# Performance work log

Measured on AMD Instinct MI355X. Metric: run time of the kernel, lower is better.

Reference implementation:

```python
import jax, jax.numpy as jnp
import numpy as np

NA, T, NUM_CIRC = 192, 80, 5
BUFFER_DIST = 0.25


def setup_inputs() -> dict:
    key = jax.random.key(0)
    k1, k2 = jax.random.split(key, 2)
    rng = np.random.default_rng(0)
    # veh_att: UNNORMALIZED (length, width) per agent
    L = rng.uniform(3.5, 5.5, NA).astype(np.float32)
    W = rng.uniform(1.6, 2.2, NA).astype(np.float32)
    rad = W / 2.0
    cent_min = -(L / 2.0) + rad
    cent_max = (L / 2.0) - rad
    # linspace of circle centers along x axis of each vehicle, (NA, num_circ)
    frac = np.linspace(0.0, 1.0, NUM_CIRC, dtype=np.float32)[None, :]
    cent_x = cent_min[:, None] + frac * (cent_max - cent_min)[:, None]
    centroids = np.stack(
        [cent_x, np.zeros_like(cent_x), np.ones_like(cent_x), np.zeros_like(cent_x)],
        axis=2,
    ).astype(np.float32)  # (NA, num_circ, 4)
    penalty_dists = (rad[:, None] + rad[None, :] + BUFFER_DIST).astype(np.float32)
    off_diag_mask = ~np.eye(NA, dtype=bool)  # single scene graph (ptr=None)
    # traj: (NA, T, 4) = (x, y, hx, hy), unnormalized world coords
    pos = jax.random.uniform(k1, (NA, T, 2), minval=-100.0, maxval=100.0)
    head = jax.random.normal(k2, (NA, T, 2))
    traj = jnp.concatenate([pos, head], axis=-1).astype(jnp.float32)
    return {
        "traj": traj,
        "centroids": jnp.asarray(centroids),
        "penalty_dists": jnp.asarray(penalty_dists),
        "off_diag_mask": jnp.asarray(off_diag_mask),
    }


def reference(traj, centroids, penalty_dists, off_diag_mask):
    # traj: (NA, T, 4); centroids: (NA, C, 4); penalty_dists/off_diag_mask: (NA, NA)
    na, t, _ = traj.shape
    xy = traj[:, :, 0:2]                     # (NA, T, 2)
    h = traj[:, :, 2:4]
    hn = h / jnp.linalg.norm(h, axis=-1, keepdims=True)  # normalized heading
    hx, hy = hn[..., 0], hn[..., 1]          # (NA, T)
    cx = centroids[..., 0]                   # (NA, C) local circle offsets
    cy = centroids[..., 1]                   # (NA, C) (zeros)
    # transform2frame(inverse=True): world = t + R(h) @ local
    wx = xy[:, :, 0:1] + hx[:, :, None] * cx[:, None, :] - hy[:, :, None] * cy[:, None, :]
    wy = xy[:, :, 1:2] + hy[:, :, None] * cx[:, None, :] + hx[:, :, None] * cy[:, None, :]
    world = jnp.stack([wx, wy], axis=-1)     # (NA, T, C, 2)
    world = jnp.transpose(world, (1, 0, 2, 3))  # (T, NA, C, 2)
    # pairwise circle distances via ||a||^2 + ||b||^2 - 2 a.b (avoids (T,NA,NA,C,C,2) diff)
    sq = jnp.sum(world * world, axis=-1)     # (T, NA, C)
    cross = jnp.einsum("tice,tjde->tijcd", world, world)  # (T, NA, NA, C, C)
    d2 = sq[:, :, None, :, None] + sq[:, None, :, None, :] - 2.0 * cross
    d = jnp.sqrt(jnp.maximum(d2, 0.0))
    min_pair_dists = jnp.min(d, axis=(3, 4))  # (T, NA, NA)
    is_colliding_mask = jnp.logical_and(
        min_pair_dists <= penalty_dists[None, :, :], off_diag_mask[None, :, :]
    )
    cur_penalties = 1.0 - min_pair_dists / penalty_dists[None, :, :]
    return cur_penalties, is_colliding_mask
```

## Files before the change

kernel.cpp:

```cpp
#include <hip/hip_runtime.h>

constexpr int NA = 192;
constexpr int TT = 80;
constexpr int NC = 5;

__device__ __forceinline__ float min3f(float a, float b, float c) {
    return fminf(fminf(a, b), c);
}

__global__ __launch_bounds__(256) void veh_coll_kernel(
    const float* __restrict__ traj,
    const float* __restrict__ cent,
    const float* __restrict__ pd,
    float* __restrict__ out_pen,
    float* __restrict__ out_mask)
{
    __shared__ float spx[NA], spy[NA], shx[NA], shy[NA];
    __shared__ float ss[NC][NA];

    const int t      = blockIdx.y;
    const int i_tile = blockIdx.x;
    const int tid    = threadIdx.x;

    if (tid < NA) {
        const float4 tr = *(const float4*)(traj + ((size_t)tid * TT + t) * 4);
        float hx = tr.z, hy = tr.w;
        const float rn = __builtin_amdgcn_rsqf(hx * hx + hy * hy);
        hx *= rn; hy *= rn;
        spx[tid] = tr.x; spy[tid] = tr.y;
        shx[tid] = hx;   shy[tid] = hy;
        #pragma unroll
        for (int c = 0; c < NC; ++c)
            ss[c][tid] = cent[((size_t)tid * NC + c) * 4];
    }
    __syncthreads();

    const int wave = tid >> 6;
    const int lane = tid & 63;

    float pix[4], piy[4], hix[4], hiy[4], s[4][NC];
    #pragma unroll
    for (int ii = 0; ii < 4; ++ii) {
        const int i = i_tile * 16 + wave * 4 + ii;
        pix[ii] = spx[i]; piy[ii] = spy[i];
        hix[ii] = shx[i]; hiy[ii] = shy[i];
        #pragma unroll
        for (int c = 0; c < NC; ++c) s[ii][c] = ss[c][i];
    }

    #pragma unroll
    for (int jb = 0; jb < 3; ++jb) {
        const int j = jb * 64 + lane;
        const float pjx = spx[j], pjy = spy[j];
        const float hjx = shx[j], hjy = shy[j];
        float r[NC];
        #pragma unroll
        for (int d = 0; d < NC; ++d) r[d] = ss[d][j];

        #pragma unroll
        for (int ii = 0; ii < 4; ++ii) {
            const int i = i_tile * 16 + wave * 4 + ii;
            const float Px = pix[ii] - pjx, Py = piy[ii] - pjy;
            const float n2 = __builtin_fmaf(Px, Px, Py * Py);
            const float al = __builtin_fmaf(Px, hix[ii], Py * hiy[ii]);
            const float be = __builtin_fmaf(Px, hjx,     Py * hjy);
            const float ga = __builtin_fmaf(hix[ii], hjx, hiy[ii] * hjy);
            const float a2 = al + al;
            const float b2 = be + be;
            const float g2 = -(ga + ga);

            float A[NC], G[NC], B[NC];
            #pragma unroll
            for (int c = 0; c < NC; ++c) {
                A[c] = __builtin_fmaf(s[ii][c], s[ii][c] + a2, n2);
                G[c] = s[ii][c] * g2;
            }
            #pragma unroll
            for (int d = 0; d < NC; ++d)
                B[d] = r[d] * (r[d] - b2);

            float mc[NC];
            #pragma unroll
            for (int c = 0; c < NC; ++c) {
                const float d0 = __builtin_fmaf(G[c], r[0], A[c] + B[0]);
                const float d1 = __builtin_fmaf(G[c], r[1], A[c] + B[1]);
                const float d2_ = __builtin_fmaf(G[c], r[2], A[c] + B[2]);
                const float d3 = __builtin_fmaf(G[c], r[3], A[c] + B[3]);
                const float d4 = __builtin_fmaf(G[c], r[4], A[c] + B[4]);
                mc[c] = fminf(min3f(d0, d1, d2_), fminf(d3, d4));
            }
            const float m = fmaxf(fminf(min3f(mc[0], mc[1], mc[2]),
                                        fminf(mc[3], mc[4])), 0.0f);

            const float dmin = __builtin_amdgcn_sqrtf(m);
            const float p    = pd[i * NA + j];
            const size_t o   = ((size_t)t * NA + i) * NA + j;
            out_pen[o]  = __builtin_fmaf(-dmin, __builtin_amdgcn_rcpf(p), 1.0f);
            out_mask[o] = ((dmin <= p) && (i != j)) ? 1.0f : 0.0f;
        }
    }
}

extern "C" void kernel_launch(void* const* d_in, const int* in_sizes, int n_in,
                              void* d_out, int out_size, void* d_ws, size_t ws_size,
                              hipStream_t stream) {
    const float* traj = (const float*)d_in[0];
    const float* cent = (const float*)d_in[1];
    const float* pd   = (const float*)d_in[2];

    float* out_pen  = (float*)d_out;
    float* out_mask = out_pen + (size_t)TT * NA * NA;

    veh_coll_kernel<<<dim3(NA / 16, TT), 256, 0, stream>>>(traj, cent, pd, out_pen, out_mask);
}
```

Baseline: 73.86 us.

## Split j dimension across grid and drop shared-memory staging

The kernel now launches a 3D grid so each block handles one 64-wide j slice instead of looping over three j slices. Each thread loads its own agent data straight from global memory (relying on cache), with no shared-memory staging and no __syncthreads barrier. This triples the number of blocks for more parallelism and latency hiding. In exchange, the i-row trajectory and centroid loads are repeated across blocks and threads, and per-thread work is smaller.

After: 76.98 us. +4.2%, slower.

```diff
diff --git a/kernel.cpp b/kernel.cpp
--- a/kernel.cpp
+++ b/kernel.cpp
@@ -15,89 +15,78 @@
     float* __restrict__ out_pen,
     float* __restrict__ out_mask)
 {
-    __shared__ float spx[NA], spy[NA], shx[NA], shy[NA];
-    __shared__ float ss[NC][NA];
-
-    const int t      = blockIdx.y;
-    const int i_tile = blockIdx.x;
-    const int tid    = threadIdx.x;
-
-    if (tid < NA) {
-        const float4 tr = *(const float4*)(traj + ((size_t)tid * TT + t) * 4);
-        float hx = tr.z, hy = tr.w;
-        const float rn = __builtin_amdgcn_rsqf(hx * hx + hy * hy);
-        hx *= rn; hy *= rn;
-        spx[tid] = tr.x; spy[tid] = tr.y;
-        shx[tid] = hx;   shy[tid] = hy;
-        #pragma unroll
-        for (int c = 0; c < NC; ++c)
-            ss[c][tid] = cent[((size_t)tid * NC + c) * 4];
-    }
-    __syncthreads();
-
+    const int t    = blockIdx.z;
+    const int tid  = threadIdx.x;
     const int wave = tid >> 6;
     const int lane = tid & 63;
+    const int i0   = blockIdx.x * 16 + wave * 4;
+    const int j    = blockIdx.y * 64 + lane;
+
+    const float4 tj = *(const float4*)(traj + ((size_t)j * TT + t) * 4);
+    const float pjx = tj.x, pjy = tj.y;
+    float hjx = tj.z, hjy = tj.w;
+    {
+        const float rn = __builtin_amdgcn_rsqf(hjx * hjx + hjy * hjy);
+        hjx *= rn; hjy *= rn;
+    }
+    float r[NC];
+    #pragma unroll
+    for (int d = 0; d < NC; ++d)
+        r[d] = cent[((size_t)j * NC + d) * 4];
 
     float pix[4], piy[4], hix[4], hiy[4], s[4][NC];
     #pragma unroll
     for (int ii = 0; ii < 4; ++ii) {
-        const int i = i_tile * 16 + wave * 4 + ii;
-        pix[ii] = spx[i]; piy[ii] = spy[i];
-        hix[ii] = shx[i]; hiy[ii] = shy[i];
+        const int i = i0 + ii;
+        const float4 ti = *(const float4*)(traj + ((size_t)i * TT + t) * 4);
+        const float rn = __builtin_amdgcn_rsqf(ti.z * ti.z + ti.w * ti.w);
+        pix[ii] = ti.x; piy[ii] = ti.y;
+        hix[ii] = ti.z * rn; hiy[ii] = ti.w * rn;
         #pragma unroll
-        for (int c = 0; c < NC; ++c) s[ii][c] = ss[c][i];
+        for (int c = 0; c < NC; ++c)
+            s[ii][c] = cent[((size_t)i * NC + c) * 4];
     }
 
     #pragma unroll
-    for (int jb = 0; jb < 3; ++jb) {
-        const int j = jb * 64 + lane;
-        const float pjx = spx[j], pjy = spy[j];
-        const float hjx = shx[j], hjy = shy[j];
-        float r[NC];
+    for (int ii = 0; ii < 4; ++ii) {
+        const int i = i0 + ii;
+        const float Px = pix[ii] - pjx, Py = piy[ii] - pjy;
+        const float n2 = __builtin_fmaf(Px, Px, Py * Py);
+        const float al = __builtin_fmaf(Px, hix[ii], Py * hiy[ii]);
+        const float be = __builtin_fmaf(Px, hjx,     Py * hjy);
+        const float ga = __builtin_fmaf(hix[ii], hjx, hiy[ii] * hjy);
+        const float a2 = al + al;
+        const float b2 = be + be;
+        const float g2 = -(ga + ga);
+
+        float A[NC], G[NC], B[NC];
         #pragma unroll
-        for (int d = 0; d < NC; ++d) r[d] = ss[d][j];
+        for (int c = 0; c < NC; ++c) {
+            A[c] = __builtin_fmaf(s[ii][c], s[ii][c] + a2, n2);
+            G[c] = s[ii][c] * g2;
+        }
+        #pragma unroll
+        for (int d = 0; d < NC; ++d)
+            B[d] = r[d] * (r[d] - b2);
 
+        float mc[NC];
         #pragma unroll
-        for (int ii = 0; ii < 4; ++ii) {
-            const int i = i_tile * 16 + wave * 4 + ii;
-            const float Px = pix[ii] - pjx, Py = piy[ii] - pjy;
-            const float n2 = __builtin_fmaf(Px, Px, Py * Py);
-            const float al = __builtin_fmaf(Px, hix[ii], Py * hiy[ii]);
-            const float be = __builtin_fmaf(Px, hjx,     Py * hjy);
-            const float ga = __builtin_fmaf(hix[ii], hjx, hiy[ii] * hjy);
-            const float a2 = al + al;
-            const float b2 = be + be;
-            const float g2 = -(ga + ga);
+        for (int c = 0; c < NC; ++c) {
+            const float d0  = __builtin_fmaf(G[c], r[0], A[c] + B[0]);
+            const float d1  = __builtin_fmaf(G[c], r[1], A[c] + B[1]);
+            const float d2_ = __builtin_fmaf(G[c], r[2], A[c] + B[2]);
+            const float d3  = __builtin_fmaf(G[c], r[3], A[c] + B[3]);
+            const float d4  = __builtin_fmaf(G[c], r[4], A[c] + B[4]);
+            mc[c] = fminf(min3f(d0, d1, d2_), fminf(d3, d4));
+        }
+        const float m = fmaxf(fminf(min3f(mc[0], mc[1], mc[2]),
+                                    fminf(mc[3], mc[4])), 0.0f);
 
-            float A[NC], G[NC], B[NC];
-            #pragma unroll
-            for (int c = 0; c < NC; ++c) {
-                A[c] = __builtin_fmaf(s[ii][c], s[ii][c] + a2, n2);
-                G[c] = s[ii][c] * g2;
-            }
-            #pragma unroll
-            for (int d = 0; d < NC; ++d)
-                B[d] = r[d] * (r[d] - b2);
-
-            float mc[NC];
-            #pragma unroll
-            for (int c = 0; c < NC; ++c) {
-                const float d0 = __builtin_fmaf(G[c], r[0], A[c] + B[0]);
-                const float d1 = __builtin_fmaf(G[c], r[1], A[c] + B[1]);
-                const float d2_ = __builtin_fmaf(G[c], r[2], A[c] + B[2]);
-                const float d3 = __builtin_fmaf(G[c], r[3], A[c] + B[3]);
-                const float d4 = __builtin_fmaf(G[c], r[4], A[c] + B[4]);
-                mc[c] = fminf(min3f(d0, d1, d2_), fminf(d3, d4));
-            }
-            const float m = fmaxf(fminf(min3f(mc[0], mc[1], mc[2]),
-                                        fminf(mc[3], mc[4])), 0.0f);
-
-            const float dmin = __builtin_amdgcn_sqrtf(m);
-            const float p    = pd[i * NA + j];
-            const size_t o   = ((size_t)t * NA + i) * NA + j;
-            out_pen[o]  = __builtin_fmaf(-dmin, __builtin_amdgcn_rcpf(p), 1.0f);
-            out_mask[o] = ((dmin <= p) && (i != j)) ? 1.0f : 0.0f;
-        }
+        const float dmin = __builtin_amdgcn_sqrtf(m);
+        const float p    = pd[i * NA + j];
+        const size_t o   = ((size_t)t * NA + i) * NA + j;
+        out_pen[o]  = __builtin_fmaf(-dmin, __builtin_amdgcn_rcpf(p), 1.0f);
+        out_mask[o] = ((dmin <= p) && (i != j)) ? 1.0f : 0.0f;
     }
 }
 
@@ -111,5 +100,6 @@
     float* out_pen  = (float*)d_out;
     float* out_mask = out_pen + (size_t)TT * NA * NA;
 
-    veh_coll_kernel<<<dim3(NA / 16, TT), 256, 0, stream>>>(traj, cent, pd, out_pen, out_mask);
+    veh_coll_kernel<<<dim3(NA / 16, NA / 64, TT), 256, 0, stream>>>(
+        traj, cent, pd, out_pen, out_mask);
 }
```
